# Optimization experiments

Hardware: AMD Instinct MI355X
Metric: run time of the kernel (lower is better)

The kernel has to match this reference:

```python
import jax, jax.numpy as jnp
import numpy as np
from jax import lax

L, B, T, C, F = 4, 4, 2048, 1024, 4096  # n_layer, batch, ctx_len, n_embd(=dim_att), dim_ffn
EPS = 1e-5


def setup_inputs() -> dict:
    key = jax.random.key(0)
    ks = jax.random.split(key, 16)
    s = 0.02
    d = {}
    d["x"] = jax.random.normal(ks[0], (B, T, C), jnp.float32)
    d["ln0_w"] = jnp.ones((C,), jnp.float32)
    d["ln0_b"] = jnp.zeros((C,), jnp.float32)
    d["ln1_w"] = jnp.ones((L, C), jnp.float32)
    d["ln1_b"] = jnp.zeros((L, C), jnp.float32)
    d["ln2_w"] = jnp.ones((L, C), jnp.float32)
    d["ln2_b"] = jnp.zeros((L, C), jnp.float32)
    d["time_decay"] = jax.random.normal(ks[1], (L, C), jnp.float32) * 0.5
    d["time_first"] = jax.random.normal(ks[2], (L, C), jnp.float32) * 0.5 + jnp.float32(np.log(0.3))
    d["tmk"] = jax.random.uniform(ks[3], (L, C), jnp.float32)
    d["tmv"] = jax.random.uniform(ks[4], (L, C), jnp.float32)
    d["tmr"] = jax.random.uniform(ks[5], (L, C), jnp.float32)
    d["Wk"] = jax.random.normal(ks[6], (L, C, C), jnp.float32) * s
    d["Wv"] = jax.random.normal(ks[7], (L, C, C), jnp.float32) * s
    d["Wr"] = jax.random.normal(ks[8], (L, C, C), jnp.float32) * s
    d["Wo"] = jax.random.normal(ks[9], (L, C, C), jnp.float32) * s
    d["cmk"] = jax.random.uniform(ks[10], (L, C), jnp.float32)
    d["cmr"] = jax.random.uniform(ks[11], (L, C), jnp.float32)
    d["Wck"] = jax.random.normal(ks[12], (L, F, C), jnp.float32) * s  # key: n_embd -> dim_ffn
    d["Wcv"] = jax.random.normal(ks[13], (L, C, F), jnp.float32) * s  # value: dim_ffn -> n_embd
    d["Wcr"] = jax.random.normal(ks[14], (L, C, C), jnp.float32) * s  # receptance
    return d


def layernorm(x, w, b):
    m = jnp.mean(x, axis=-1, keepdims=True)
    v = jnp.var(x, axis=-1, keepdims=True)
    return (x - m) * lax.rsqrt(v + EPS) * w + b


def time_shift(x):
    # ZeroPad2d((0,0,1,-1)): shift sequence right by one, zero at t=0
    return jnp.pad(x, ((0, 0), (1, 0), (0, 0)))[:, :-1]


def wkv(time_decay, time_first, k, v):
    # numerically-stable RWKV-4 WKV recurrence; k,v: [B,T,C]
    w = -jnp.exp(time_decay)  # [C]
    u = time_first            # [C]
    kt = jnp.swapaxes(k, 0, 1)  # [T,B,C]
    vt = jnp.swapaxes(v, 0, 1)
    Bn, Cn = k.shape[0], k.shape[2]
    init = (jnp.zeros((Bn, Cn), k.dtype), jnp.zeros((Bn, Cn), k.dtype),
            jnp.full((Bn, Cn), -1e38, k.dtype))

    def step(carry, kv):
        aa, bb, pp = carry
        kk, vv = kv
        ww = u + kk
        qq = jnp.maximum(pp, ww)
        e1 = jnp.exp(pp - qq)
        e2 = jnp.exp(ww - qq)
        out = (e1 * aa + e2 * vv) / (e1 * bb + e2)
        ww2 = pp + w
        qq2 = jnp.maximum(ww2, kk)
        e1b = jnp.exp(ww2 - qq2)
        e2b = jnp.exp(kk - qq2)
        return (e1b * aa + e2b * vv, e1b * bb + e2b, qq2), out

    _, out = lax.scan(step, init, (kt, vt))
    return jnp.swapaxes(out, 0, 1)  # [B,T,C]


def reference(x, ln0_w, ln0_b, ln1_w, ln1_b, ln2_w, ln2_b, time_decay, time_first,
              tmk, tmv, tmr, Wk, Wv, Wr, Wo, cmk, cmr, Wck, Wcv, Wcr):
    x = layernorm(x, ln0_w, ln0_b)  # ln0 on layer 0
    for l in range(L):
        # --- TimeMix ---
        h = layernorm(x, ln1_w[l], ln1_b[l])
        hh = time_shift(h)
        xk = h * tmk[l] + hh * (1 - tmk[l])
        xv = h * tmv[l] + hh * (1 - tmv[l])
        xr = h * tmr[l] + hh * (1 - tmr[l])
        k = jnp.einsum('btc,oc->bto', xk, Wk[l])
        v = jnp.einsum('btc,oc->bto', xv, Wv[l])
        sr = jax.nn.sigmoid(jnp.einsum('btc,oc->bto', xr, Wr[l]))
        rwkv = sr * wkv(time_decay[l], time_first[l], k, v)
        x = x + jnp.einsum('bto,co->btc', rwkv, Wo[l])
        # --- ChannelMix ---
        h = layernorm(x, ln2_w[l], ln2_b[l])
        hh = time_shift(h)
        xk = h * cmk[l] + hh * (1 - cmk[l])
        xr = h * cmr[l] + hh * (1 - cmr[l])
        kf = jnp.einsum('btc,fc->btf', xk, Wck[l])
        kf = jnp.square(jax.nn.relu(kf))
        kv = jnp.einsum('btf,cf->btc', kf, Wcv[l])
        x = x + jax.nn.sigmoid(jnp.einsum('btc,oc->bto', xr, Wcr[l])) * kv
    return x
```

## Files before the change

kernel.cpp:

```cpp
#include <hip/hip_runtime.h>
#include <cstdint>

#define TT 2048
#define CCH 1024
#define FFD 4096
#define EPSV 1e-5f
#define NCHK 32
#define CHKL 64

typedef __attribute__((ext_vector_type(4))) float floatx4;
typedef __attribute__((ext_vector_type(8))) short shortx8;

__device__ __forceinline__ unsigned short f32_to_bf16(float f){
  union { float f; unsigned int u; } x; x.f = f;
  unsigned int r = x.u + 0x7fffu + ((x.u >> 16) & 1u);
  return (unsigned short)(r >> 16);
}
__device__ __forceinline__ float bf16_to_f32(unsigned short h){
  union { unsigned int u; float f; } x; x.u = ((unsigned int)h) << 16;
  return x.f;
}
__device__ __forceinline__ float wave_sum(float v){
  #pragma unroll
  for (int o = 32; o > 0; o >>= 1) v += __shfl_down(v, o, 64);
  return v;
}
__device__ __forceinline__ void async16(const void* g, void* l){
  __builtin_amdgcn_global_load_lds((const __attribute__((address_space(1))) void*)g,
                                   (__attribute__((address_space(3))) void*)l, 16, 0, 0);
}

struct CvtArgs {
  const float* s[7];
  unsigned short* d[7];
  int n4[7];
};
__global__ __launch_bounds__(256) void cvt7_kernel(CvtArgs a){
  const int seg = blockIdx.y;
  const float* __restrict__ s = a.s[seg];
  unsigned short* __restrict__ d = a.d[seg];
  const int n4 = a.n4[seg];
  for (int i = blockIdx.x * 256 + threadIdx.x; i < n4; i += gridDim.x * 256) {
    float4 v = ((const float4*)s)[i];
    union { unsigned short u[4]; uint2 p; } o;
    o.u[0] = f32_to_bf16(v.x); o.u[1] = f32_to_bf16(v.y);
    o.u[2] = f32_to_bf16(v.z); o.u[3] = f32_to_bf16(v.w);
    *(uint2*)&d[(long)i * 4] = o.p;
  }
}

__global__ __launch_bounds__(256) void ln0_kernel(const float* __restrict__ xin,
    const float* __restrict__ w, const float* __restrict__ b, float* __restrict__ xo){
  const int row = blockIdx.x, tid = threadIdx.x;
  const float* xr = xin + (long)row * CCH;
  float c4[4]; float s = 0.f, s2 = 0.f;
  #pragma unroll
  for (int j = 0; j < 4; j++){ c4[j] = xr[tid + j*256]; s += c4[j]; s2 += c4[j]*c4[j]; }
  s = wave_sum(s); s2 = wave_sum(s2);
  __shared__ float red[2][4];
  const int wid = tid >> 6, lane = tid & 63;
  if (lane == 0){ red[0][wid] = s; red[1][wid] = s2; }
  __syncthreads();
  const float S  = red[0][0]+red[0][1]+red[0][2]+red[0][3];
  const float S2 = red[1][0]+red[1][1]+red[1][2]+red[1][3];
  const float inv = 1.f / CCH;
  const float m = S * inv;
  const float rs = rsqrtf(S2 * inv - m*m + EPSV);
  float* xout = xo + (long)row * CCH;
  #pragma unroll
  for (int j = 0; j < 4; j++){ int c = tid + j*256; xout[c] = (c4[j]-m)*rs*w[c] + b[c]; }
}

template<int NOUT>
__global__ __launch_bounds__(256) void ln_mix(
    const float* __restrict__ x,
    const float* __restrict__ lw, const float* __restrict__ lb,
    const float* __restrict__ mk, const float* __restrict__ mv, const float* __restrict__ mr,
    unsigned short* __restrict__ xk, unsigned short* __restrict__ xv, unsigned short* __restrict__ xr)
{
  const int row = blockIdx.x;
  const int t = row & (TT - 1);
  const int tid = threadIdx.x;
  const float* xc = x + (long)row * CCH;
  const float* xp = xc - CCH;
  float c4[4], p4[4];
  float s1=0.f, s2=0.f, s3=0.f, s4=0.f;
  #pragma unroll
  for (int j = 0; j < 4; j++){
    const int c = tid + j*256;
    c4[j] = xc[c];
    p4[j] = (t > 0) ? xp[c] : 0.f;
    s1 += c4[j]; s2 += c4[j]*c4[j];
    s3 += p4[j]; s4 += p4[j]*p4[j];
  }
  s1 = wave_sum(s1); s2 = wave_sum(s2); s3 = wave_sum(s3); s4 = wave_sum(s4);
  __shared__ float red[4][4];
  const int wid = tid >> 6, lane = tid & 63;
  if (lane == 0){ red[wid][0]=s1; red[wid][1]=s2; red[wid][2]=s3; red[wid][3]=s4; }
  __syncthreads();
  const float S1 = red[0][0]+red[1][0]+red[2][0]+red[3][0];
  const float S2 = red[0][1]+red[1][1]+red[2][1]+red[3][1];
  const float S3 = red[0][2]+red[1][2]+red[2][2]+red[3][2];
  const float S4 = red[0][3]+red[1][3]+red[2][3]+red[3][3];
  const float inv = 1.f / CCH;
  const float m1 = S1*inv; const float r1 = rsqrtf(S2*inv - m1*m1 + EPSV);
  const float m0 = S3*inv; const float r0 = rsqrtf(S4*inv - m0*m0 + EPSV);
  #pragma unroll
  for (int j = 0; j < 4; j++){
    const int c = tid + j*256;
    const long o = (long)row * CCH + c;
    const float wv = lw[c], bv = lb[c];
    const float h  = (c4[j]-m1)*r1*wv + bv;
    const float hp = (t > 0) ? ((p4[j]-m0)*r0*wv + bv) : 0.f;
    const float a = mk[c]; xk[o] = f32_to_bf16(h*a + hp*(1.f-a));
    if (NOUT == 3){ const float q = mv[c]; xv[o] = f32_to_bf16(h*q + hp*(1.f-q)); }
    const float g = mr[c]; xr[o] = f32_to_bf16(h*g + hp*(1.f-g));
  }
}

__global__ __launch_bounds__(256) void wkv_pass1(
    const unsigned short* __restrict__ kin, const unsigned short* __restrict__ vin,
    const float* __restrict__ td,
    float* __restrict__ sta, float* __restrict__ stb, float* __restrict__ stp)
{
  const int c = blockIdx.x * 256 + threadIdx.x;
  const int chunk = blockIdx.y, b = blockIdx.z;
  const float w = -__expf(td[c]);
  const long base = ((long)b * TT + (long)chunk * CHKL) * CCH + c;
  float aa = 0.f, bb = 0.f, pp = -1e38f;
  for (int t0 = 0; t0 < CHKL; t0 += 8) {
    float kr[8], vr[8];
    #pragma unroll
    for (int j = 0; j < 8; j++){
      const long o = base + (long)(t0 + j) * CCH;
      kr[j] = bf16_to_f32(kin[o]);
      vr[j] = bf16_to_f32(vin[o]);
    }
    #pragma unroll
    for (int j = 0; j < 8; j++){
      const float kk = kr[j], vv = vr[j];
      const float ww2 = pp + w;
      const float qq2 = fmaxf(ww2, kk);
      const float e1b = __expf(ww2 - qq2), e2b = __expf(kk - qq2);
      aa = e1b*aa + e2b*vv; bb = e1b*bb + e2b; pp = qq2;
    }
  }
  const long si = (long)chunk * 4096 + b * CCH + c;
  sta[si] = aa; stb[si] = bb; stp[si] = pp;
}

__global__ __launch_bounds__(256) void wkv_combine(
    const float* __restrict__ td,
    const float* __restrict__ sta, const float* __restrict__ stb, const float* __restrict__ stp,
    float* __restrict__ ina, float* __restrict__ inb, float* __restrict__ inp)
{
  const int idx = blockIdx.x * 256 + threadIdx.x;
  const int c = idx & (CCH - 1);
  const float wn = -__expf(td[c]) * (float)CHKL;
  float a = 0.f, b = 0.f, p = -1e38f;
  for (int j0 = 0; j0 < NCHK; j0 += 8) {
    float la[8], lb[8], lp[8];
    #pragma unroll
    for (int j = 0; j < 8; j++){
      const long si = (long)(j0 + j) * 4096 + idx;
      la[j] = sta[si]; lb[j] = stb[si]; lp[j] = stp[si];
    }
    #pragma unroll
    for (int j = 0; j < 8; j++){
      const long si = (long)(j0 + j) * 4096 + idx;
      ina[si] = a; inb[si] = b; inp[si] = p;
      const float pd = p + wn;
      const float q = fmaxf(pd, lp[j]);
      const float e1 = __expf(pd - q), e2 = __expf(lp[j] - q);
      a = e1*a + e2*la[j]; b = e1*b + e2*lb[j]; p = q;
    }
  }
}

__global__ __launch_bounds__(256) void wkv_pass2(
    const unsigned short* __restrict__ kin, const unsigned short* __restrict__ vin,
    const unsigned short* __restrict__ srin,
    const float* __restrict__ td, const float* __restrict__ tf,
    const float* __restrict__ ina, const float* __restrict__ inb, const float* __restrict__ inp,
    unsigned short* __restrict__ out)
{
  const int c = blockIdx.x * 256 + threadIdx.x;
  const int chunk = blockIdx.y, b = blockIdx.z;
  const float w = -__expf(td[c]);
  const float u = tf[c];
  const long si = (long)chunk * 4096 + b * CCH + c;
  float aa = ina[si], bb = inb[si], pp = inp[si];
  const long base = ((long)b * TT + (long)chunk * CHKL) * CCH + c;
  for (int t0 = 0; t0 < CHKL; t0 += 8) {
    float kr[8], vr[8], sr[8];
    #pragma unroll
    for (int j = 0; j < 8; j++){
      const long o = base + (long)(t0 + j) * CCH;
      kr[j] = bf16_to_f32(kin[o]);
      vr[j] = bf16_to_f32(vin[o]);
      sr[j] = bf16_to_f32(srin[o]);
    }
    #pragma unroll
    for (int j = 0; j < 8; j++){
      const float kk = kr[j], vv = vr[j];
      const float ww = u + kk;
      const float qq = fmaxf(pp, ww);
      const float e1 = __expf(pp - qq), e2 = __expf(ww - qq);
      const float outv = (e1*aa + e2*vv) / (e1*bb + e2);
      const float ww2 = pp + w;
      const float qq2 = fmaxf(ww2, kk);
      const float e1b = __expf(ww2 - qq2), e2b = __expf(kk - qq2);
      aa = e1b*aa + e2b*vv; bb = e1b*bb + e2b; pp = qq2;
      out[base + (long)(t0 + j) * CCH] = f32_to_bf16(sr[j] * outv);
    }
  }
}

#define BM 128
#define BN 128
#define BK 64

enum { EP_BF16 = 0, EP_SIG = 1, EP_RELU2 = 2, EP_ADD = 3, EP_MULADD = 4, EP_KVR = 5 };

template<int EPI>
__global__ __launch_bounds__(256) void gemm_bt(
    const unsigned short* __restrict__ A,
    const unsigned short* __restrict__ W,
    const int N, const int K,
    unsigned short* __restrict__ outb,
    float* __restrict__ xres,
    const unsigned short* __restrict__ rr)
{
  if (EPI == EP_KVR) {
    const long z = blockIdx.z;
    const long Mfull = (long)gridDim.x * BM;
    A    += z * Mfull * K;
    W    += z * (long)N * K;
    outb += z * Mfull * N;
  }
  __shared__ unsigned short lA[BM * BK];
  __shared__ unsigned short lW[BN * BK];
  const int tid = threadIdx.x;
  const int bm = blockIdx.x, bn = blockIdx.y;
  const int wid = tid >> 6, lane = tid & 63;
  const int wm = (wid >> 1) * 64, wn = (wid & 1) * 64;
  const int quad = lane >> 4, r16 = lane & 15;

  const int srow = tid >> 3;
  const int scol = (tid & 7) ^ (srow & 7);
  const unsigned short* Ag = A + ((long)(bm * BM + srow)) * K + scol * 8;
  const unsigned short* Wg = W + ((long)(bn * BN + srow)) * K + scol * 8;
  const long rs32 = (long)32 * K;

  const int sw0 = ((quad)     ^ (r16 & 7)) * 8;
  const int sw1 = ((4 + quad) ^ (r16 & 7)) * 8;

  const floatx4 zf = {0.f, 0.f, 0.f, 0.f};
  floatx4 acc[4][4];
  #pragma unroll
  for (int i = 0; i < 4; i++)
    #pragma unroll
    for (int j = 0; j < 4; j++) acc[i][j] = zf;

  for (int k0 = 0; k0 < K; k0 += BK) {
    __syncthreads();
    #pragma unroll
    for (int i = 0; i < 4; i++) {
      async16(Ag + (long)i * rs32 + k0, &lA[(i * 256 + wid * 64) * 8]);
      async16(Wg + (long)i * rs32 + k0, &lW[(i * 256 + wid * 64) * 8]);
    }
    __syncthreads();
    #pragma unroll
    for (int kk = 0; kk < 2; kk++) {
      const int sw = kk ? sw1 : sw0;
      shortx8 af[4], bf[4];
      #pragma unroll
      for (int m = 0; m < 4; m++) af[m] = *(const shortx8*)&lA[(wm + m*16 + r16) * 64 + sw];
      #pragma unroll
      for (int n = 0; n < 4; n++) bf[n] = *(const shortx8*)&lW[(wn + n*16 + r16) * 64 + sw];
      #pragma unroll
      for (int m = 0; m < 4; m++)
        #pragma unroll
        for (int n = 0; n < 4; n++)
          acc[m][n] = __builtin_amdgcn_mfma_f32_16x16x32_bf16(af[m], bf[n], acc[m][n], 0, 0, 0);
    }
  }

  const int colBase = bn * BN + wn + r16;
  #pragma unroll
  for (int m = 0; m < 4; m++) {
    const int rowBase = bm * BM + wm + m * 16 + quad * 4;
    #pragma unroll
    for (int n = 0; n < 4; n++) {
      const int col = colBase + n * 16;
      #pragma unroll
      for (int r = 0; r < 4; r++) {
        const long idx = (long)(rowBase + r) * N + col;
        const float val = acc[m][n][r];
        if (EPI == EP_BF16)      outb[idx] = f32_to_bf16(val);
        else if (EPI == EP_KVR)  outb[idx] = (blockIdx.z == 2)
                                   ? f32_to_bf16(1.f / (1.f + __expf(-val)))
                                   : f32_to_bf16(val);
        else if (EPI == EP_SIG)  outb[idx] = f32_to_bf16(1.f / (1.f + __expf(-val)));
        else if (EPI == EP_RELU2){ const float t = val > 0.f ? val : 0.f; outb[idx] = f32_to_bf16(t * t); }
        else if (EPI == EP_ADD)  xres[idx] += val;
        else                     xres[idx] = fmaf(bf16_to_f32(rr[idx]), val, xres[idx]);
      }
    }
  }
}

extern "C" void kernel_launch(void* const* d_in, const int* in_sizes, int n_in,
                              void* d_out, int out_size, void* d_ws, size_t ws_size,
                              hipStream_t stream)
{
  const float* x_in       = (const float*)d_in[0];
  const float* ln0_w      = (const float*)d_in[1];
  const float* ln0_b      = (const float*)d_in[2];
  const float* ln1_w      = (const float*)d_in[3];
  const float* ln1_b      = (const float*)d_in[4];
  const float* ln2_w      = (const float*)d_in[5];
  const float* ln2_b      = (const float*)d_in[6];
  const float* time_decay = (const float*)d_in[7];
  const float* time_first = (const float*)d_in[8];
  const float* tmk        = (const float*)d_in[9];
  const float* tmv        = (const float*)d_in[10];
  const float* tmr        = (const float*)d_in[11];
  const float* Wk         = (const float*)d_in[12];
  const float* Wv         = (const float*)d_in[13];
  const float* Wr         = (const float*)d_in[14];
  const float* Wo         = (const float*)d_in[15];
  const float* cmk        = (const float*)d_in[16];
  const float* cmr        = (const float*)d_in[17];
  const float* Wck        = (const float*)d_in[18];
  const float* Wcv        = (const float*)d_in[19];
  const float* Wcr        = (const float*)d_in[20];
  float* x = (float*)d_out;

  const int M = 4 * TT;
  const long lCC = (long)CCH * CCH;
  const long lFC = (long)FFD * CCH;
  const long MC  = (long)M * CCH;

  unsigned short* wsl  = (unsigned short*)d_ws;
  unsigned short* wkb  = wsl;
  unsigned short* wvb  = wkb + lCC;
  unsigned short* wrb  = wvb + lCC;
  unsigned short* wob  = wrb + lCC;
  unsigned short* wcrb = wob + lCC;
  unsigned short* wckb = wcrb + lCC;
  unsigned short* wcvb = wckb + lFC;
  unsigned short* xk   = wcvb + lFC;
  unsigned short* xv   = xk + MC;
  unsigned short* xr   = xv + MC;
  unsigned short* kbuf = xr + MC;
  unsigned short* vbuf = kbuf + MC;
  unsigned short* sbuf = vbuf + MC;
  unsigned short* kfb  = kbuf;
  unsigned short* rrb  = kbuf + (long)M * FFD;

  float* sta = (float*)xk;
  float* stb = sta + (long)NCHK * 4096;
  float* stp = stb + (long)NCHK * 4096;
  float* ina = stp + (long)NCHK * 4096;
  float* inb = ina + (long)NCHK * 4096;
  float* inp = inb + (long)NCHK * 4096;

  ln0_kernel<<<M, 256, 0, stream>>>(x_in, ln0_w, ln0_b, x);

  const dim3 g1(M / BM, CCH / BN);
  const dim3 g2(M / BM, FFD / BN);
  const dim3 gkvr(M / BM, CCH / BN, 3);
  const dim3 gw(CCH / 256, NCHK, 4);

  for (int l = 0; l < 4; l++) {
    CvtArgs ca;
    ca.s[0] = Wk  + (long)l * lCC; ca.d[0] = wkb;  ca.n4[0] = (int)(lCC / 4);
    ca.s[1] = Wv  + (long)l * lCC; ca.d[1] = wvb;  ca.n4[1] = (int)(lCC / 4);
    ca.s[2] = Wr  + (long)l * lCC; ca.d[2] = wrb;  ca.n4[2] = (int)(lCC / 4);
    ca.s[3] = Wo  + (long)l * lCC; ca.d[3] = wob;  ca.n4[3] = (int)(lCC / 4);
    ca.s[4] = Wcr + (long)l * lCC; ca.d[4] = wcrb; ca.n4[4] = (int)(lCC / 4);
    ca.s[5] = Wck + (long)l * lFC; ca.d[5] = wckb; ca.n4[5] = (int)(lFC / 4);
    ca.s[6] = Wcv + (long)l * lFC; ca.d[6] = wcvb; ca.n4[6] = (int)(lFC / 4);
    cvt7_kernel<<<dim3(512, 7), 256, 0, stream>>>(ca);

    const float* td_l = time_decay + l*CCH;
    const float* tf_l = time_first + l*CCH;

    ln_mix<3><<<M, 256, 0, stream>>>(x, ln1_w + l*CCH, ln1_b + l*CCH,
                                     tmk + l*CCH, tmv + l*CCH, tmr + l*CCH, xk, xv, xr);
    gemm_bt<EP_KVR><<<gkvr, 256, 0, stream>>>(xk, wkb, CCH, CCH, kbuf, nullptr, nullptr);
    wkv_pass1 <<<gw, 256, 0, stream>>>(kbuf, vbuf, td_l, sta, stb, stp);
    wkv_combine<<<16, 256, 0, stream>>>(td_l, sta, stb, stp, ina, inb, inp);
    wkv_pass2 <<<gw, 256, 0, stream>>>(kbuf, vbuf, sbuf, td_l, tf_l, ina, inb, inp, xv);
    gemm_bt<EP_ADD ><<<g1, 256, 0, stream>>>(xv, wob, CCH, CCH, nullptr, x, nullptr);

    ln_mix<2><<<M, 256, 0, stream>>>(x, ln2_w + l*CCH, ln2_b + l*CCH,
                                     cmk + l*CCH, nullptr, cmr + l*CCH, xk, nullptr, xr);
    gemm_bt<EP_SIG   ><<<g1, 256, 0, stream>>>(xr, wcrb, CCH, CCH, rrb, nullptr, nullptr);
    gemm_bt<EP_RELU2 ><<<g2, 256, 0, stream>>>(xk, wckb, FFD, CCH, kfb, nullptr, nullptr);
    gemm_bt<EP_MULADD><<<g1, 256, 0, stream>>>(kfb, wcvb, CCH, FFD, nullptr, x, rrb);
  }
}
```

Before: 1.711 ms.

## Double-buffer GEMM LDS with BK=32 stages and merge receptance into FFN-key launch

The GEMM main loop now uses two 32-wide K stages in LDS. The next tile is fetched asynchronously while MFMAs run on the current one, so each step needs one barrier instead of two. The LDS swizzle is redone for the 32-wide tile. The channel-mix receptance GEMM (sigmoid) and the FFN key GEMM (relu²) are merged into one launch using a z dimension, and blocks beyond the receptance's width exit early. This saves a launch and lets the two GEMMs share the machine, but the smaller BK halves the work per barrier and the merged grid wastes many blocks that only exit.

```diff
diff --git a/kernel.cpp b/kernel.cpp
--- a/kernel.cpp
+++ b/kernel.cpp
@@ -218,42 +218,62 @@
 
 #define BM 128
 #define BN 128
-#define BK 64
-
-enum { EP_BF16 = 0, EP_SIG = 1, EP_RELU2 = 2, EP_ADD = 3, EP_MULADD = 4, EP_KVR = 5 };
+
+enum { EP_BF16 = 0, EP_SIG = 1, EP_RELU2 = 2, EP_ADD = 3, EP_MULADD = 4, EP_KVR = 5, EP_FFN1 = 6 };
 
 template<int EPI>
 __global__ __launch_bounds__(256) void gemm_bt(
     const unsigned short* __restrict__ A,
     const unsigned short* __restrict__ W,
-    const int N, const int K,
+    int N, const int K,
     unsigned short* __restrict__ outb,
     float* __restrict__ xres,
-    const unsigned short* __restrict__ rr)
-{
+    const unsigned short* __restrict__ rr,
+    const unsigned short* __restrict__ A2,
+    const unsigned short* __restrict__ W2,
+    unsigned short* __restrict__ outb2,
+    const int N2)
+{
+  const int bm = blockIdx.x, bn = blockIdx.y;
+  bool sig = false;
   if (EPI == EP_KVR) {
     const long z = blockIdx.z;
     const long Mfull = (long)gridDim.x * BM;
     A    += z * Mfull * K;
     W    += z * (long)N * K;
     outb += z * Mfull * N;
-  }
-  __shared__ unsigned short lA[BM * BK];
-  __shared__ unsigned short lW[BN * BK];
+    sig = (blockIdx.z == 2);
+  }
+  if (EPI == EP_FFN1) {
+    if (blockIdx.z == 1) {
+      if (bn >= N2 / BN) return;
+      A = A2; W = W2; outb = outb2; N = N2; sig = true;
+    }
+  }
+  __shared__ unsigned short lA[2 * 4096];
+  __shared__ unsigned short lW[2 * 4096];
   const int tid = threadIdx.x;
-  const int bm = blockIdx.x, bn = blockIdx.y;
   const int wid = tid >> 6, lane = tid & 63;
   const int wm = (wid >> 1) * 64, wn = (wid & 1) * 64;
   const int quad = lane >> 4, r16 = lane & 15;
 
-  const int srow = tid >> 3;
-  const int scol = (tid & 7) ^ (srow & 7);
-  const unsigned short* Ag = A + ((long)(bm * BM + srow)) * K + scol * 8;
-  const unsigned short* Wg = W + ((long)(bn * BN + srow)) * K + scol * 8;
-  const long rs32 = (long)32 * K;
-
-  const int sw0 = ((quad)     ^ (r16 & 7)) * 8;
-  const int sw1 = ((4 + quad) ^ (r16 & 7)) * 8;
+  int rowS[2], chkS[2];
+  #pragma unroll
+  for (int i = 0; i < 2; i++) {
+    const int P = i * 256 + tid;
+    const int line = P >> 3, slot = P & 7;
+    const int sp = slot ^ (line & 7);
+    rowS[i] = 2 * line + (sp >> 2);
+    chkS[i] = sp & 3;
+  }
+  const unsigned short* Ag0 = A + (long)(bm * BM + rowS[0]) * K + chkS[0] * 8;
+  const unsigned short* Ag1 = A + (long)(bm * BM + rowS[1]) * K + chkS[1] * 8;
+  const unsigned short* Wg0 = W + (long)(bn * BN + rowS[0]) * K + chkS[0] * 8;
+  const unsigned short* Wg1 = W + (long)(bn * BN + rowS[1]) * K + chkS[1] * 8;
+  const int ldsP0 = tid * 8;
+  const int ldsP1 = (256 + tid) * 8;
+
+  const int laneOff = (r16 >> 1) * 64 + (((quad + ((r16 & 1) << 2)) ^ (r16 >> 1)) * 8);
 
   const floatx4 zf = {0.f, 0.f, 0.f, 0.f};
   floatx4 acc[4][4];
@@ -262,28 +282,32 @@
     #pragma unroll
     for (int j = 0; j < 4; j++) acc[i][j] = zf;
 
-  for (int k0 = 0; k0 < K; k0 += BK) {
+  const int nst = K >> 5;
+  int buf = 0;
+  async16(Ag0, &lA[ldsP0]); async16(Ag1, &lA[ldsP1]);
+  async16(Wg0, &lW[ldsP0]); async16(Wg1, &lW[ldsP1]);
+  __syncthreads();
+  for (int s = 0; s < nst; s++) {
+    const int nb = buf ^ 1;
+    if (s + 1 < nst) {
+      const int k0 = (s + 1) << 5;
+      async16(Ag0 + k0, &lA[nb * 4096 + ldsP0]);
+      async16(Ag1 + k0, &lA[nb * 4096 + ldsP1]);
+      async16(Wg0 + k0, &lW[nb * 4096 + ldsP0]);
+      async16(Wg1 + k0, &lW[nb * 4096 + ldsP1]);
+    }
+    shortx8 af[4], bf[4];
+    #pragma unroll
+    for (int m = 0; m < 4; m++) af[m] = *(const shortx8*)&lA[buf * 4096 + (wm + m * 16) * 32 + laneOff];
+    #pragma unroll
+    for (int n = 0; n < 4; n++) bf[n] = *(const shortx8*)&lW[buf * 4096 + (wn + n * 16) * 32 + laneOff];
+    #pragma unroll
+    for (int m = 0; m < 4; m++)
+      #pragma unroll
+      for (int n = 0; n < 4; n++)
+        acc[m][n] = __builtin_amdgcn_mfma_f32_16x16x32_bf16(af[m], bf[n], acc[m][n], 0, 0, 0);
     __syncthreads();
-    #pragma unroll
-    for (int i = 0; i < 4; i++) {
-      async16(Ag + (long)i * rs32 + k0, &lA[(i * 256 + wid * 64) * 8]);
-      async16(Wg + (long)i * rs32 + k0, &lW[(i * 256 + wid * 64) * 8]);
-    }
-    __syncthreads();
-    #pragma unroll
-    for (int kk = 0; kk < 2; kk++) {
-      const int sw = kk ? sw1 : sw0;
-      shortx8 af[4], bf[4];
-      #pragma unroll
-      for (int m = 0; m < 4; m++) af[m] = *(const shortx8*)&lA[(wm + m*16 + r16) * 64 + sw];
-      #pragma unroll
-      for (int n = 0; n < 4; n++) bf[n] = *(const shortx8*)&lW[(wn + n*16 + r16) * 64 + sw];
-      #pragma unroll
-      for (int m = 0; m < 4; m++)
-        #pragma unroll
-        for (int n = 0; n < 4; n++)
-          acc[m][n] = __builtin_amdgcn_mfma_f32_16x16x32_bf16(af[m], bf[n], acc[m][n], 0, 0, 0);
-    }
+    buf = nb;
   }
 
   const int colBase = bn * BN + wn + r16;
@@ -297,14 +321,15 @@
       for (int r = 0; r < 4; r++) {
         const long idx = (long)(rowBase + r) * N + col;
         const float val = acc[m][n][r];
-        if (EPI == EP_BF16)      outb[idx] = f32_to_bf16(val);
-        else if (EPI == EP_KVR)  outb[idx] = (blockIdx.z == 2)
-                                   ? f32_to_bf16(1.f / (1.f + __expf(-val)))
-                                   : f32_to_bf16(val);
-        else if (EPI == EP_SIG)  outb[idx] = f32_to_bf16(1.f / (1.f + __expf(-val)));
-        else if (EPI == EP_RELU2){ const float t = val > 0.f ? val : 0.f; outb[idx] = f32_to_bf16(t * t); }
+        if (EPI == EP_KVR)       outb[idx] = sig ? f32_to_bf16(1.f / (1.f + __expf(-val)))
+                                                 : f32_to_bf16(val);
+        else if (EPI == EP_FFN1) {
+          if (sig) outb[idx] = f32_to_bf16(1.f / (1.f + __expf(-val)));
+          else     { const float t = val > 0.f ? val : 0.f; outb[idx] = f32_to_bf16(t * t); }
+        }
         else if (EPI == EP_ADD)  xres[idx] += val;
-        else                     xres[idx] = fmaf(bf16_to_f32(rr[idx]), val, xres[idx]);
+        else if (EPI == EP_MULADD) xres[idx] = fmaf(bf16_to_f32(rr[idx]), val, xres[idx]);
+        else                     outb[idx] = f32_to_bf16(val);
       }
     }
   }
@@ -369,8 +394,8 @@
   ln0_kernel<<<M, 256, 0, stream>>>(x_in, ln0_w, ln0_b, x);
 
   const dim3 g1(M / BM, CCH / BN);
-  const dim3 g2(M / BM, FFD / BN);
   const dim3 gkvr(M / BM, CCH / BN, 3);
+  const dim3 gffn(M / BM, FFD / BN, 2);
   const dim3 gw(CCH / 256, NCHK, 4);
 
   for (int l = 0; l < 4; l++) {
@@ -389,16 +414,19 @@
 
     ln_mix<3><<<M, 256, 0, stream>>>(x, ln1_w + l*CCH, ln1_b + l*CCH,
                                      tmk + l*CCH, tmv + l*CCH, tmr + l*CCH, xk, xv, xr);
-    gemm_bt<EP_KVR><<<gkvr, 256, 0, stream>>>(xk, wkb, CCH, CCH, kbuf, nullptr, nullptr);
+    gemm_bt<EP_KVR><<<gkvr, 256, 0, stream>>>(xk, wkb, CCH, CCH, kbuf, nullptr, nullptr,
+                                              nullptr, nullptr, nullptr, 0);
     wkv_pass1 <<<gw, 256, 0, stream>>>(kbuf, vbuf, td_l, sta, stb, stp);
     wkv_combine<<<16, 256, 0, stream>>>(td_l, sta, stb, stp, ina, inb, inp);
     wkv_pass2 <<<gw, 256, 0, stream>>>(kbuf, vbuf, sbuf, td_l, tf_l, ina, inb, inp, xv);
-    gemm_bt<EP_ADD ><<<g1, 256, 0, stream>>>(xv, wob, CCH, CCH, nullptr, x, nullptr);
+    gemm_bt<EP_ADD ><<<g1, 256, 0, stream>>>(xv, wob, CCH, CCH, nullptr, x, nullptr,
+                                             nullptr, nullptr, nullptr, 0);
 
     ln_mix<2><<<M, 256, 0, stream>>>(x, ln2_w + l*CCH, ln2_b + l*CCH,
                                      cmk + l*CCH, nullptr, cmr + l*CCH, xk, nullptr, xr);
-    gemm_bt<EP_SIG   ><<<g1, 256, 0, stream>>>(xr, wcrb, CCH, CCH, rrb, nullptr, nullptr);
-    gemm_bt<EP_RELU2 ><<<g2, 256, 0, stream>>>(xk, wckb, FFD, CCH, kfb, nullptr, nullptr);
-    gemm_bt<EP_MULADD><<<g1, 256, 0, stream>>>(kfb, wcvb, CCH, FFD, nullptr, x, rrb);
-  }
-}
+    gemm_bt<EP_FFN1><<<gffn, 256, 0, stream>>>(xk, wckb, FFD, CCH, kfb, nullptr, nullptr,
+                                               xr, wcrb, rrb, CCH);
+    gemm_bt<EP_MULADD><<<g1, 256, 0, stream>>>(kfb, wcvb, CCH, FFD, nullptr, x, rrb,
+                                               nullptr, nullptr, nullptr, 0);
+  }
+}
```

Measured after the change: 1.778 ms. 3.9% more time.
